# Performance work log

Hardware: AMD Instinct MI355X
Metric: run time of the kernel (lower is better)

Reference implementation:

```python
import jax, jax.numpy as jnp
import numpy as np

N_CELL, N_NET, N_GCELL = 50000, 10000, 20000
E = 100000
D = 32   # hidden_node = hidden_net = hidden_hanna = out_node = out_net
DP = 16  # hidden_pin = hidden_edge feats


def setup_inputs() -> dict:
    key = jax.random.key(0)
    ks = jax.random.split(key, 21)
    f = jax.random.normal
    ri = lambda k, n: jax.random.randint(k, (E,), 0, n, dtype=jnp.int32)
    return {
        'node_feat': f(ks[0], (N_CELL, D), jnp.float32),
        'net_feat': f(ks[1], (N_NET, D), jnp.float32),
        'pin_feat': f(ks[2], (E, DP), jnp.float32),
        'hanna_feat': f(ks[3], (N_GCELL, D), jnp.float32),
        'edge_feat': f(ks[4], (E, DP), jnp.float32),
        'pins_src': ri(ks[5], N_CELL), 'pins_dst': ri(ks[6], N_NET),
        'pinned_src': ri(ks[7], N_NET), 'pinned_dst': ri(ks[8], N_CELL),
        'connect_src': ri(ks[9], N_GCELL), 'connect_dst': ri(ks[10], N_GCELL),
        'pt_src': ri(ks[11], N_CELL), 'pt_dst': ri(ks[12], N_GCELL),
        'pf_src': ri(ks[13], N_GCELL), 'pf_dst': ri(ks[14], N_CELL),
        'W_net': f(ks[15], (D, D)) * 0.1, 'b_net': jnp.zeros((D,), jnp.float32),
        'W_topo': f(ks[16], (DP, D * D)) * 0.1, 'b_topo': jnp.zeros((D * D,), jnp.float32),
        'W_pins': f(ks[17], (D, D)) * 0.1, 'b_pins': jnp.zeros((D,), jnp.float32),
        'W_connect': f(ks[18], (D, D)) * 0.1, 'b_connect': jnp.zeros((D,), jnp.float32),
        'W_pt': f(ks[19], (D, D)) * 0.1, 'b_pt': jnp.zeros((D,), jnp.float32),
        'b_pinned': jnp.zeros((D,), jnp.float32), 'b_pf': jnp.zeros((D,), jnp.float32),
    }


def _deg(idx, n):
    # clamped degree, as DGL clamps to min 1
    return jnp.maximum(jax.ops.segment_sum(jnp.ones_like(idx, jnp.float32), idx, n), 1.0)


def graph_conv(h_src, W, b, src, dst, n_src, n_dst):
    # DGL GraphConv with norm='both': D_out^{-1/2} gather -> sum -> D_in^{-1/2}, then W, b
    feat = (h_src * _deg(src, n_src)[:, None] ** -0.5) @ W
    agg = jax.ops.segment_sum(feat[src], dst, n_dst)
    return agg * _deg(dst, n_dst)[:, None] ** -0.5 + b


def nn_conv(h_src, efeat, W_topo, b_topo, bias, src, dst, n_dst):
    # DGL NNConv (aggregator='mean'): per-edge weight from edge_func, mean over in-edges
    d_in = h_src.shape[1]
    w = (efeat @ W_topo + b_topo).reshape(-1, d_in, bias.shape[0])  # (E, d_in, d_out)
    m = jnp.einsum('ei,eio->eo', h_src[src], w)
    return jax.ops.segment_sum(m, dst, n_dst) / _deg(dst, n_dst)[:, None] + bias


def reference(node_feat, net_feat, pin_feat, hanna_feat, edge_feat,
              pins_src, pins_dst, pinned_src, pinned_dst, connect_src, connect_dst,
              pt_src, pt_dst, pf_src, pf_dst,
              W_net, b_net, W_topo, b_topo, W_pins, b_pins,
              W_connect, b_connect, W_pt, b_pt, b_pinned, b_pf):
    # 'pins': cell -> net (GraphConv)
    h_net = graph_conv(node_feat, W_pins, b_pins, pins_src, pins_dst, N_CELL, N_NET)
    # 'pinned': net -> cell (NNConv) + 'point-from': gcell -> cell (NNConv); agg='sum'
    h_cell = (nn_conv(net_feat, pin_feat, W_topo, b_topo, b_pinned, pinned_src, pinned_dst, N_CELL)
              + nn_conv(hanna_feat, edge_feat, W_topo, b_topo, b_pf, pf_src, pf_dst, N_CELL))
    # 'connect': gcell -> gcell + 'point-to': cell -> gcell (GraphConvs); agg='sum'
    h_gcell = (graph_conv(hanna_feat, W_connect, b_connect, connect_src, connect_dst, N_GCELL, N_GCELL)
               + graph_conv(node_feat, W_pt, b_pt, pt_src, pt_dst, N_CELL, N_GCELL))
    return (h_cell, h_net + net_feat @ W_net + b_net, h_gcell)
```

## Files before the change

kernel.cpp:

```cpp
#include <hip/hip_runtime.h>

typedef unsigned short u16;
typedef unsigned int u32;

#define NC 50000
#define NN 10000
#define NG 20000
#define NE 100000
#define NSCAN 150016
#define NBLK 74


__device__ __forceinline__ float bflo(u32 a) { return __uint_as_float(a << 16); }
__device__ __forceinline__ float bfhi(u32 a) { return __uint_as_float(a & 0xFFFF0000u); }
__device__ __forceinline__ u16 fbf(float f) {
  u32 u = __float_as_uint(f);
  return (u16)((u + 0x7FFFu + ((u >> 16) & 1u)) >> 16);
}

__device__ __forceinline__ float nn_msg(int e, int s, const float* __restrict__ ef,
                                        const u16* __restrict__ T,
                                        const float* __restrict__ C, int o) {
  const float4* efp = reinterpret_cast<const float4*>(ef + (size_t)e * 16);
  float4 ea = efp[0], eb = efp[1], ec = efp[2], ed = efp[3];
  const uint4* tp = reinterpret_cast<const uint4*>(T + (size_t)s * 512 + o * 16);
  uint4 ta = tp[0], tb = tp[1];
  float m = C[(size_t)s * 32 + o];
  m += ea.x * bflo(ta.x) + ea.y * bfhi(ta.x) + ea.z * bflo(ta.y) + ea.w * bfhi(ta.y);
  m += eb.x * bflo(ta.z) + eb.y * bfhi(ta.z) + eb.z * bflo(ta.w) + eb.w * bfhi(ta.w);
  m += ec.x * bflo(tb.x) + ec.y * bfhi(tb.x) + ec.z * bflo(tb.y) + ec.w * bfhi(tb.y);
  m += ed.x * bflo(tb.z) + ed.y * bfhi(tb.z) + ed.z * bflo(tb.w) + ed.w * bfhi(tb.w);
  return m;
}

__global__ __launch_bounds__(512) void k_front(
    const float* __restrict__ feat_net, const float* __restrict__ feat_han,
    const float* __restrict__ W_topo, const float* __restrict__ b_topo,
    u16* __restrict__ T_net, u16* __restrict__ T_han,
    float* __restrict__ C_net, float* __restrict__ C_han,
    const int* __restrict__ pins_src, const int* __restrict__ pins_dst,
    const int* __restrict__ pinned_dst, const int* __restrict__ pf_dst,
    const int* __restrict__ connect_src, const int* __restrict__ connect_dst,
    const int* __restrict__ pt_src, const int* __restrict__ pt_dst,
    int* __restrict__ hist, int* __restrict__ srccnt) {
  int b = blockIdx.x;
  if (b < 938) {
    bool han = b >= 313;
    const float* feat = han ? feat_han : feat_net;
    u16* T = han ? T_han : T_net;
    int n = han ? NG : NN;
    int blk = han ? b - 313 : b;
    int j = threadIdx.x;
    int p = j & 15, o = j >> 4;
    float w[32];
#pragma unroll
    for (int i = 0; i < 32; i++) w[i] = W_topo[p * 1024 + i * 32 + o];
    int s0 = blk * 32;
    int s1 = min(s0 + 32, n);
    int sn = s0;
    for (; sn + 1 < s1; sn += 2) {
      const float* h0 = feat + (size_t)sn * 32;
      const float* h1 = h0 + 32;
      float a0 = 0.f, a1 = 0.f;
#pragma unroll
      for (int i = 0; i < 32; i++) {
        a0 += h0[i] * w[i];
        a1 += h1[i] * w[i];
      }
      T[(size_t)sn * 512 + j] = fbf(a0);
      T[(size_t)(sn + 1) * 512 + j] = fbf(a1);
    }
    if (sn < s1) {
      const float* h0 = feat + (size_t)sn * 32;
      float a0 = 0.f;
#pragma unroll
      for (int i = 0; i < 32; i++) a0 += h0[i] * w[i];
      T[(size_t)sn * 512 + j] = fbf(a0);
    }
    return;
  }
  if (b < 2813) {
    int t = (b - 938) * 512 + threadIdx.x;
    int s2 = t >> 5, o = t & 31;
    bool han = s2 >= NN;
    const float* feat = han ? feat_han : feat_net;
    float* C = han ? C_han : C_net;
    int s = han ? s2 - NN : s2;
    float acc = 0.f;
#pragma unroll 8
    for (int i = 0; i < 32; i++)
      acc += feat[(size_t)s * 32 + i] * b_topo[i * 32 + o];
    C[(size_t)s * 32 + o] = acc;
    return;
  }
  int e = (b - 2813) * 512 + threadIdx.x;
  if (e >= NE) return;
  atomicAdd(&hist[pins_dst[e]], 1);
  atomicAdd(&hist[10000 + connect_dst[e]], 1);
  atomicAdd(&hist[30000 + pt_dst[e]], 1);
  atomicAdd(&hist[50000 + pinned_dst[e]], 1);
  atomicAdd(&hist[100000 + pf_dst[e]], 1);
  atomicAdd(&srccnt[pins_src[e]], 1);
  atomicAdd(&srccnt[50000 + connect_src[e]], 1);
  atomicAdd(&srccnt[70000 + pt_src[e]], 1);
}

__global__ __launch_bounds__(256) void k_scan1(
    const int* __restrict__ cnt, int* __restrict__ bsum) {
  __shared__ int sm[256];
  int b = blockIdx.x, tid = threadIdx.x;
  int base = b * 2048 + tid * 8;
  int tot = 0;
#pragma unroll
  for (int j = 0; j < 8; j++) {
    int i = base + j;
    tot += (i < NSCAN) ? cnt[i] : 0;
  }
  sm[tid] = tot;
  __syncthreads();
  for (int off = 128; off > 0; off >>= 1) {
    if (tid < off) sm[tid] += sm[tid + off];
    __syncthreads();
  }
  if (tid == 0) bsum[b] = sm[0];
}

__global__ __launch_bounds__(256) void k_scan3(
    const int* __restrict__ cnt, const int* __restrict__ bsum,
    int* __restrict__ bases) {
  __shared__ int sm[256];
  __shared__ int carry;
  int b = blockIdx.x, tid = threadIdx.x;
  if (tid == 0) {
    int run = 0;
    for (int i = 0; i < NBLK; i++) {
      if (i == b) break;
      run += bsum[i];
    }
    carry = run;
  }
  int base = b * 2048 + tid * 8;
  int v[8];
  int tot = 0;
#pragma unroll
  for (int j = 0; j < 8; j++) {
    int i = base + j;
    v[j] = (i < NSCAN) ? cnt[i] : 0;
    tot += v[j];
  }
  sm[tid] = tot;
  __syncthreads();
  for (int off = 1; off < 256; off <<= 1) {
    int add = (tid >= off) ? sm[tid - off] : 0;
    __syncthreads();
    sm[tid] += add;
    __syncthreads();
  }
  int excl = sm[tid] - tot + carry;
#pragma unroll
  for (int j = 0; j < 8; j++) {
    int i = base + j;
    if (i < NSCAN) bases[i] = excl;
    excl += v[j];
  }
}

__global__ __launch_bounds__(512) void k_fill(
    const int* __restrict__ pins_dst, const int* __restrict__ connect_dst,
    const int* __restrict__ pt_dst, const int* __restrict__ pinned_dst,
    const int* __restrict__ pf_dst,
    const int* __restrict__ bases, int* __restrict__ cursor,
    int* __restrict__ idx_all) {
  int t = blockIdx.x * 512 + threadIdx.x;
  if (t >= 5 * NE) return;
  int r = t / NE, e = t - r * NE;
  const int* dsts = r == 0 ? pins_dst : r == 1 ? connect_dst
                   : r == 2 ? pt_dst : r == 3 ? pinned_dst : pf_dst;
  int off = r == 0 ? 0 : r == 1 ? 10000 : r == 2 ? 30000 : r == 3 ? 50000 : 100000;
  int g = off + dsts[e];
  int pos = atomicAdd(&cursor[g], 1);
  idx_all[bases[g] + pos] = e;
}

__global__ __launch_bounds__(512) void k_gc_gather(
    const int* __restrict__ hist, const int* __restrict__ bases,
    const int* __restrict__ idx_all, const int* __restrict__ srccnt,
    const int* __restrict__ pins_src, const int* __restrict__ connect_src,
    const int* __restrict__ pt_src,
    const float* __restrict__ node_feat, const float* __restrict__ hanna_feat,
    float* __restrict__ S_net, float* __restrict__ S_conn, float* __restrict__ S_pt) {
  int t = blockIdx.x * 512 + threadIdx.x;
  int rr = t >> 5, o = t & 31;
  int rel = (rr >= 10000) + (rr >= 30000);
  const int* srcarr = rel == 0 ? pins_src : rel == 1 ? connect_src : pt_src;
  const float* feat = (rel == 1) ? hanna_feat : node_feat;
  const int* scnt = srccnt + (rel == 0 ? 0 : rel == 1 ? 50000 : 70000);
  float* S = rel == 0 ? S_net + (size_t)rr * 32
           : rel == 1 ? S_conn + (size_t)(rr - 10000) * 32
                      : S_pt + (size_t)(rr - 30000) * 32;
  int base = bases[rr], deg = hist[rr];
  float acc = 0.f;
  int k = 0;
  for (; k + 1 < deg; k += 2) {
    int ea = idx_all[base + k], eb = idx_all[base + k + 1];
    int sa = srcarr[ea], sb = srcarr[eb];
    float wa = rsqrtf(fmaxf((float)scnt[sa], 1.f));
    float wb = rsqrtf(fmaxf((float)scnt[sb], 1.f));
    acc += feat[(size_t)sa * 32 + o] * wa + feat[(size_t)sb * 32 + o] * wb;
  }
  if (k < deg) {
    int e = idx_all[base + k];
    int s = srcarr[e];
    acc += feat[(size_t)s * 32 + o] * rsqrtf(fmaxf((float)scnt[s], 1.f));
  }
  S[o] = acc;
}

__global__ __launch_bounds__(512) void k_tail(
    const int* __restrict__ hist, const int* __restrict__ bases,
    const int* __restrict__ idx_all,
    const int* __restrict__ pinned_src, const int* __restrict__ pf_src,
    const float* __restrict__ pin_feat, const float* __restrict__ edge_feat,
    const u16* __restrict__ T_net, const u16* __restrict__ T_han,
    const float* __restrict__ C_net, const float* __restrict__ C_han,
    const float* __restrict__ b_pinned, const float* __restrict__ b_pf,
    const float* __restrict__ S_net, const float* __restrict__ net_feat,
    const float* __restrict__ W_pins, const float* __restrict__ b_pins,
    const float* __restrict__ W_net, const float* __restrict__ b_net,
    const float* __restrict__ S_conn, const float* __restrict__ S_pt,
    const float* __restrict__ W_connect, const float* __restrict__ b_connect,
    const float* __restrict__ W_pt, const float* __restrict__ b_pt,
    float* __restrict__ out) {
  __shared__ float Wa[1024], Wb[1024];
  int b = blockIdx.x;
  if (b < 3125) {
    int t = b * 512 + threadIdx.x;
    int d = t >> 5, o = t & 31;
    float a0 = 0.f, a1 = 0.f;
    {
      int g = 50000 + d;
      int base = bases[g], deg = hist[g];
      int k = 0;
      for (; k + 1 < deg; k += 2) {
        int ea = idx_all[base + k], eb = idx_all[base + k + 1];
        int sa = pinned_src[ea], sb = pinned_src[eb];
        a0 += nn_msg(ea, sa, pin_feat, T_net, C_net, o) +
              nn_msg(eb, sb, pin_feat, T_net, C_net, o);
      }
      if (k < deg) {
        int e = idx_all[base + k];
        a0 += nn_msg(e, pinned_src[e], pin_feat, T_net, C_net, o);
      }
      a0 /= fmaxf((float)deg, 1.f);
    }
    {
      int g = 100000 + d;
      int base = bases[g], deg = hist[g];
      int k = 0;
      for (; k + 1 < deg; k += 2) {
        int ea = idx_all[base + k], eb = idx_all[base + k + 1];
        int sa = pf_src[ea], sb = pf_src[eb];
        a1 += nn_msg(ea, sa, edge_feat, T_han, C_han, o) +
              nn_msg(eb, sb, edge_feat, T_han, C_han, o);
      }
      if (k < deg) {
        int e = idx_all[base + k];
        a1 += nn_msg(e, pf_src[e], edge_feat, T_han, C_han, o);
      }
      a1 /= fmaxf((float)deg, 1.f);
    }
    out[(size_t)d * 32 + o] = a0 + a1 + b_pinned[o] + b_pf[o];
    return;
  }
  if (b < 3750) {
    for (int k = threadIdx.x; k < 1024; k += 512) {
      Wa[k] = W_pins[k];
      Wb[k] = W_net[k];
    }
    __syncthreads();
    int t = (b - 3125) * 512 + threadIdx.x;
    int r = t >> 5, o = t & 31;
    float a1 = 0.f, a2 = 0.f;
#pragma unroll 8
    for (int i = 0; i < 32; i++) {
      a1 += S_net[(size_t)r * 32 + i] * Wa[i * 32 + o];
      a2 += net_feat[(size_t)r * 32 + i] * Wb[i * 32 + o];
    }
    out[1600000 + t] = a1 * rsqrtf(fmaxf((float)hist[r], 1.f)) + b_pins[o] +
                       a2 + b_net[o];
    return;
  }
  for (int k = threadIdx.x; k < 1024; k += 512) {
    Wa[k] = W_connect[k];
    Wb[k] = W_pt[k];
  }
  __syncthreads();
  int t = (b - 3750) * 512 + threadIdx.x;
  int r = t >> 5, o = t & 31;
  float a1 = 0.f, a2 = 0.f;
#pragma unroll 8
  for (int i = 0; i < 32; i++) {
    a1 += S_conn[(size_t)r * 32 + i] * Wa[i * 32 + o];
    a2 += S_pt[(size_t)r * 32 + i] * Wb[i * 32 + o];
  }
  out[1920000 + t] = a1 * rsqrtf(fmaxf((float)hist[10000 + r], 1.f)) + b_connect[o] +
                     a2 * rsqrtf(fmaxf((float)hist[30000 + r], 1.f)) + b_pt[o];
}

extern "C" void kernel_launch(void* const* d_in, const int* in_sizes, int n_in,
                              void* d_out, int out_size, void* d_ws, size_t ws_size,
                              hipStream_t stream) {
  const float* node_feat  = (const float*)d_in[0];
  const float* net_feat   = (const float*)d_in[1];
  const float* pin_feat   = (const float*)d_in[2];
  const float* hanna_feat = (const float*)d_in[3];
  const float* edge_feat  = (const float*)d_in[4];
  const int* pins_src    = (const int*)d_in[5];
  const int* pins_dst    = (const int*)d_in[6];
  const int* pinned_src  = (const int*)d_in[7];
  const int* pinned_dst  = (const int*)d_in[8];
  const int* connect_src = (const int*)d_in[9];
  const int* connect_dst = (const int*)d_in[10];
  const int* pt_src      = (const int*)d_in[11];
  const int* pt_dst      = (const int*)d_in[12];
  const int* pf_src      = (const int*)d_in[13];
  const int* pf_dst      = (const int*)d_in[14];
  const float* W_net     = (const float*)d_in[15];
  const float* b_net     = (const float*)d_in[16];
  const float* W_topo    = (const float*)d_in[17];
  const float* b_topo    = (const float*)d_in[18];
  const float* W_pins    = (const float*)d_in[19];
  const float* b_pins    = (const float*)d_in[20];
  const float* W_connect = (const float*)d_in[21];
  const float* b_connect = (const float*)d_in[22];
  const float* W_pt      = (const float*)d_in[23];
  const float* b_pt      = (const float*)d_in[24];
  const float* b_pinned  = (const float*)d_in[25];
  const float* b_pf      = (const float*)d_in[26];
  float* out = (float*)d_out;

  int* wi = (int*)d_ws;
  int* hist    = wi + 0;
  int* cursor  = wi + 150016;
  int* srccnt  = wi + 300032;
  int* bases   = wi + 420032;
  int* bsum    = wi + 570064;
  int* idx_all = wi + 570192;
  float* wf = (float*)d_ws;
  float* S_net  = wf + 1070192;
  float* S_conn = wf + 1390192;
  float* S_pt   = wf + 2030192;
  float* C_net  = wf + 2670192;
  float* C_han  = wf + 2990192;
  u16* T_net = (u16*)((char*)d_ws + 14520832);
  u16* T_han = (u16*)((char*)d_ws + 14520832 + 10240000);

  hipMemsetAsync(d_ws, 0, 420032 * sizeof(int), stream);

  k_front<<<3009, 512, 0, stream>>>(
      net_feat, hanna_feat, W_topo, b_topo, T_net, T_han, C_net, C_han,
      pins_src, pins_dst, pinned_dst, pf_dst, connect_src, connect_dst,
      pt_src, pt_dst, hist, srccnt);

  k_scan1<<<NBLK, 256, 0, stream>>>(hist, bsum);
  k_scan3<<<NBLK, 256, 0, stream>>>(hist, bsum, bases);

  k_fill<<<(5 * NE + 511) / 512, 512, 0, stream>>>(
      pins_dst, connect_dst, pt_dst, pinned_dst, pf_dst, bases, cursor, idx_all);

  k_gc_gather<<<3125, 512, 0, stream>>>(
      hist, bases, idx_all, srccnt, pins_src, connect_src, pt_src,
      node_feat, hanna_feat, S_net, S_conn, S_pt);

  k_tail<<<5000, 512, 0, stream>>>(
      hist, bases, idx_all, pinned_src, pf_src, pin_feat, edge_feat,
      T_net, T_han, C_net, C_han, b_pinned, b_pf,
      S_net, net_feat, W_pins, b_pins, W_net, b_net,
      S_conn, S_pt, W_connect, b_connect, W_pt, b_pt, out);
}
```

Before: 303.9 us.

## Store source ids and norm weights in CSR; tile topo transform through shared memory

The fill kernel now writes CSR entries as int2 pairs, with the source index and a precomputed rsqrt degree weight for GraphConv relations, and edge id plus source for NNConv relations. This removes the dependent idx→src→srccnt gather chains in the gather and tail kernels. The topo-transform front blocks stage 64 feature rows in shared memory, compute two outputs per thread and write packed bf16 pairs, which cuts the block count. In exchange the CSR doubles in size, the fill kernel does more work, and the workspace layout is shifted.

```diff
diff --git a/kernel.cpp b/kernel.cpp
--- a/kernel.cpp
+++ b/kernel.cpp
@@ -44,43 +44,55 @@
     const int* __restrict__ pt_src, const int* __restrict__ pt_dst,
     int* __restrict__ hist, int* __restrict__ srccnt) {
   int b = blockIdx.x;
-  if (b < 938) {
-    bool han = b >= 313;
-    const float* feat = han ? feat_han : feat_net;
-    u16* T = han ? T_han : T_net;
-    int n = han ? NG : NN;
-    int blk = han ? b - 313 : b;
-    int j = threadIdx.x;
-    int p = j & 15, o = j >> 4;
-    float w[32];
-#pragma unroll
-    for (int i = 0; i < 32; i++) w[i] = W_topo[p * 1024 + i * 32 + o];
-    int s0 = blk * 32;
-    int s1 = min(s0 + 32, n);
-    int sn = s0;
-    for (; sn + 1 < s1; sn += 2) {
-      const float* h0 = feat + (size_t)sn * 32;
-      const float* h1 = h0 + 32;
+  int tid = threadIdx.x;
+  if (b < 469) {
+    __shared__ float hs[64][32];
+    int nd0 = b * 64;
+    {
+      int idx = tid * 4;
+      int nl = idx >> 5, i = idx & 31;
+      int ng = nd0 + nl;
+      int ngc = min(ng, 29999);
+      const float* rp = (ngc < NN) ? feat_net + (size_t)ngc * 32
+                                   : feat_han + (size_t)(ngc - NN) * 32;
+      *reinterpret_cast<float4*>(&hs[nl][i]) =
+          *reinterpret_cast<const float4*>(rp + i);
+    }
+    int jj = tid & 255;
+    int j0 = jj * 2, j1 = j0 + 1;
+    int p0 = j0 & 15, o0 = j0 >> 4;
+    int p1 = j1 & 15, o1 = j1 >> 4;
+    float w0[32], w1[32];
+#pragma unroll
+    for (int i = 0; i < 32; i++) {
+      w0[i] = W_topo[p0 * 1024 + i * 32 + o0];
+      w1[i] = W_topo[p1 * 1024 + i * 32 + o1];
+    }
+    __syncthreads();
+    int g = tid >> 8;
+#pragma unroll 4
+    for (int n = 0; n < 32; n++) {
+      int nl = g * 32 + n;
       float a0 = 0.f, a1 = 0.f;
 #pragma unroll
       for (int i = 0; i < 32; i++) {
-        a0 += h0[i] * w[i];
-        a1 += h1[i] * w[i];
-      }
-      T[(size_t)sn * 512 + j] = fbf(a0);
-      T[(size_t)(sn + 1) * 512 + j] = fbf(a1);
-    }
-    if (sn < s1) {
-      const float* h0 = feat + (size_t)sn * 32;
-      float a0 = 0.f;
-#pragma unroll
-      for (int i = 0; i < 32; i++) a0 += h0[i] * w[i];
-      T[(size_t)sn * 512 + j] = fbf(a0);
+        float h = hs[nl][i];
+        a0 += h * w0[i];
+        a1 += h * w1[i];
+      }
+      int s = nd0 + nl;
+      if (s < 30000) {
+        u32 pk = (u32)fbf(a0) | ((u32)fbf(a1) << 16);
+        u32* dst = (s < NN)
+            ? reinterpret_cast<u32*>(T_net + (size_t)s * 512 + j0)
+            : reinterpret_cast<u32*>(T_han + (size_t)(s - NN) * 512 + j0);
+        *dst = pk;
+      }
     }
     return;
   }
-  if (b < 2813) {
-    int t = (b - 938) * 512 + threadIdx.x;
+  if (b < 2344) {
+    int t = (b - 469) * 512 + tid;
     int s2 = t >> 5, o = t & 31;
     bool han = s2 >= NN;
     const float* feat = han ? feat_han : feat_net;
@@ -93,7 +105,7 @@
     C[(size_t)s * 32 + o] = acc;
     return;
   }
-  int e = (b - 2813) * 512 + threadIdx.x;
+  int e = (b - 2344) * 512 + tid;
   if (e >= NE) return;
   atomicAdd(&hist[pins_dst[e]], 1);
   atomicAdd(&hist[10000 + connect_dst[e]], 1);
@@ -133,10 +145,7 @@
   int b = blockIdx.x, tid = threadIdx.x;
   if (tid == 0) {
     int run = 0;
-    for (int i = 0; i < NBLK; i++) {
-      if (i == b) break;
-      run += bsum[i];
-    }
+    for (int i = 0; i < b; i++) run += bsum[i];
     carry = run;
   }
   int base = b * 2048 + tid * 8;
@@ -166,35 +175,45 @@
 }
 
 __global__ __launch_bounds__(512) void k_fill(
-    const int* __restrict__ pins_dst, const int* __restrict__ connect_dst,
-    const int* __restrict__ pt_dst, const int* __restrict__ pinned_dst,
-    const int* __restrict__ pf_dst,
+    const int* __restrict__ pins_src, const int* __restrict__ pins_dst,
+    const int* __restrict__ connect_src, const int* __restrict__ connect_dst,
+    const int* __restrict__ pt_src, const int* __restrict__ pt_dst,
+    const int* __restrict__ pinned_src, const int* __restrict__ pinned_dst,
+    const int* __restrict__ pf_src, const int* __restrict__ pf_dst,
+    const int* __restrict__ srccnt,
     const int* __restrict__ bases, int* __restrict__ cursor,
-    int* __restrict__ idx_all) {
+    int2* __restrict__ csr_gc, int2* __restrict__ csr_nn) {
   int t = blockIdx.x * 512 + threadIdx.x;
   if (t >= 5 * NE) return;
-  int r = t / NE, e = t - r * NE;
+  int r = (t >= NE) + (t >= 2 * NE) + (t >= 3 * NE) + (t >= 4 * NE);
+  int e = t - r * NE;
+  const int* srcs = r == 0 ? pins_src : r == 1 ? connect_src
+                   : r == 2 ? pt_src : r == 3 ? pinned_src : pf_src;
   const int* dsts = r == 0 ? pins_dst : r == 1 ? connect_dst
                    : r == 2 ? pt_dst : r == 3 ? pinned_dst : pf_dst;
   int off = r == 0 ? 0 : r == 1 ? 10000 : r == 2 ? 30000 : r == 3 ? 50000 : 100000;
+  int s = srcs[e];
   int g = off + dsts[e];
   int pos = atomicAdd(&cursor[g], 1);
-  idx_all[bases[g] + pos] = e;
+  int cpos = bases[g] + pos;
+  if (r < 3) {
+    int soff = r == 0 ? 0 : r == 1 ? 50000 : 70000;
+    float w = rsqrtf(fmaxf((float)srccnt[soff + s], 1.f));
+    csr_gc[cpos] = make_int2(s, __float_as_int(w));
+  } else {
+    csr_nn[cpos - 300000] = make_int2(e, s);
+  }
 }
 
 __global__ __launch_bounds__(512) void k_gc_gather(
     const int* __restrict__ hist, const int* __restrict__ bases,
-    const int* __restrict__ idx_all, const int* __restrict__ srccnt,
-    const int* __restrict__ pins_src, const int* __restrict__ connect_src,
-    const int* __restrict__ pt_src,
+    const int2* __restrict__ csr_gc,
     const float* __restrict__ node_feat, const float* __restrict__ hanna_feat,
     float* __restrict__ S_net, float* __restrict__ S_conn, float* __restrict__ S_pt) {
   int t = blockIdx.x * 512 + threadIdx.x;
   int rr = t >> 5, o = t & 31;
   int rel = (rr >= 10000) + (rr >= 30000);
-  const int* srcarr = rel == 0 ? pins_src : rel == 1 ? connect_src : pt_src;
   const float* feat = (rel == 1) ? hanna_feat : node_feat;
-  const int* scnt = srccnt + (rel == 0 ? 0 : rel == 1 ? 50000 : 70000);
   float* S = rel == 0 ? S_net + (size_t)rr * 32
            : rel == 1 ? S_conn + (size_t)(rr - 10000) * 32
                       : S_pt + (size_t)(rr - 30000) * 32;
@@ -202,24 +221,20 @@
   float acc = 0.f;
   int k = 0;
   for (; k + 1 < deg; k += 2) {
-    int ea = idx_all[base + k], eb = idx_all[base + k + 1];
-    int sa = srcarr[ea], sb = srcarr[eb];
-    float wa = rsqrtf(fmaxf((float)scnt[sa], 1.f));
-    float wb = rsqrtf(fmaxf((float)scnt[sb], 1.f));
-    acc += feat[(size_t)sa * 32 + o] * wa + feat[(size_t)sb * 32 + o] * wb;
+    int2 pa = csr_gc[base + k], pb = csr_gc[base + k + 1];
+    acc += feat[(size_t)pa.x * 32 + o] * __int_as_float(pa.y) +
+           feat[(size_t)pb.x * 32 + o] * __int_as_float(pb.y);
   }
   if (k < deg) {
-    int e = idx_all[base + k];
-    int s = srcarr[e];
-    acc += feat[(size_t)s * 32 + o] * rsqrtf(fmaxf((float)scnt[s], 1.f));
+    int2 pa = csr_gc[base + k];
+    acc += feat[(size_t)pa.x * 32 + o] * __int_as_float(pa.y);
   }
   S[o] = acc;
 }
 
 __global__ __launch_bounds__(512) void k_tail(
     const int* __restrict__ hist, const int* __restrict__ bases,
-    const int* __restrict__ idx_all,
-    const int* __restrict__ pinned_src, const int* __restrict__ pf_src,
+    const int2* __restrict__ csr_nn,
     const float* __restrict__ pin_feat, const float* __restrict__ edge_feat,
     const u16* __restrict__ T_net, const u16* __restrict__ T_han,
     const float* __restrict__ C_net, const float* __restrict__ C_han,
@@ -239,33 +254,31 @@
     float a0 = 0.f, a1 = 0.f;
     {
       int g = 50000 + d;
-      int base = bases[g], deg = hist[g];
+      int base = bases[g] - 300000, deg = hist[g];
       int k = 0;
       for (; k + 1 < deg; k += 2) {
-        int ea = idx_all[base + k], eb = idx_all[base + k + 1];
-        int sa = pinned_src[ea], sb = pinned_src[eb];
-        a0 += nn_msg(ea, sa, pin_feat, T_net, C_net, o) +
-              nn_msg(eb, sb, pin_feat, T_net, C_net, o);
+        int2 ea = csr_nn[base + k], eb = csr_nn[base + k + 1];
+        a0 += nn_msg(ea.x, ea.y, pin_feat, T_net, C_net, o) +
+              nn_msg(eb.x, eb.y, pin_feat, T_net, C_net, o);
       }
       if (k < deg) {
-        int e = idx_all[base + k];
-        a0 += nn_msg(e, pinned_src[e], pin_feat, T_net, C_net, o);
+        int2 ea = csr_nn[base + k];
+        a0 += nn_msg(ea.x, ea.y, pin_feat, T_net, C_net, o);
       }
       a0 /= fmaxf((float)deg, 1.f);
     }
     {
       int g = 100000 + d;
-      int base = bases[g], deg = hist[g];
+      int base = bases[g] - 300000, deg = hist[g];
       int k = 0;
       for (; k + 1 < deg; k += 2) {
-        int ea = idx_all[base + k], eb = idx_all[base + k + 1];
-        int sa = pf_src[ea], sb = pf_src[eb];
-        a1 += nn_msg(ea, sa, edge_feat, T_han, C_han, o) +
-              nn_msg(eb, sb, edge_feat, T_han, C_han, o);
+        int2 ea = csr_nn[base + k], eb = csr_nn[base + k + 1];
+        a1 += nn_msg(ea.x, ea.y, edge_feat, T_han, C_han, o) +
+              nn_msg(eb.x, eb.y, edge_feat, T_han, C_han, o);
       }
       if (k < deg) {
-        int e = idx_all[base + k];
-        a1 += nn_msg(e, pf_src[e], edge_feat, T_han, C_han, o);
+        int2 ea = csr_nn[base + k];
+        a1 += nn_msg(ea.x, ea.y, edge_feat, T_han, C_han, o);
       }
       a1 /= fmaxf((float)deg, 1.f);
     }
@@ -345,19 +358,20 @@
   int* srccnt  = wi + 300032;
   int* bases   = wi + 420032;
   int* bsum    = wi + 570064;
-  int* idx_all = wi + 570192;
+  int2* csr_gc = (int2*)(wi + 570192);
+  int2* csr_nn = (int2*)(wi + 1170192);
   float* wf = (float*)d_ws;
-  float* S_net  = wf + 1070192;
-  float* S_conn = wf + 1390192;
-  float* S_pt   = wf + 2030192;
-  float* C_net  = wf + 2670192;
-  float* C_han  = wf + 2990192;
-  u16* T_net = (u16*)((char*)d_ws + 14520832);
-  u16* T_han = (u16*)((char*)d_ws + 14520832 + 10240000);
+  float* S_net  = wf + 1570192;
+  float* S_conn = wf + 1890192;
+  float* S_pt   = wf + 2530192;
+  float* C_net  = wf + 3170192;
+  float* C_han  = wf + 3490192;
+  u16* T_net = (u16*)((char*)d_ws + 16520832);
+  u16* T_han = (u16*)((char*)d_ws + 16520832 + 10240000);
 
   hipMemsetAsync(d_ws, 0, 420032 * sizeof(int), stream);
 
-  k_front<<<3009, 512, 0, stream>>>(
+  k_front<<<2540, 512, 0, stream>>>(
       net_feat, hanna_feat, W_topo, b_topo, T_net, T_han, C_net, C_han,
       pins_src, pins_dst, pinned_dst, pf_dst, connect_src, connect_dst,
       pt_src, pt_dst, hist, srccnt);
@@ -366,14 +380,15 @@
   k_scan3<<<NBLK, 256, 0, stream>>>(hist, bsum, bases);
 
   k_fill<<<(5 * NE + 511) / 512, 512, 0, stream>>>(
-      pins_dst, connect_dst, pt_dst, pinned_dst, pf_dst, bases, cursor, idx_all);
+      pins_src, pins_dst, connect_src, connect_dst, pt_src, pt_dst,
+      pinned_src, pinned_dst, pf_src, pf_dst, srccnt, bases, cursor,
+      csr_gc, csr_nn);
 
   k_gc_gather<<<3125, 512, 0, stream>>>(
-      hist, bases, idx_all, srccnt, pins_src, connect_src, pt_src,
-      node_feat, hanna_feat, S_net, S_conn, S_pt);
+      hist, bases, csr_gc, node_feat, hanna_feat, S_net, S_conn, S_pt);
 
   k_tail<<<5000, 512, 0, stream>>>(
-      hist, bases, idx_all, pinned_src, pf_src, pin_feat, edge_feat,
+      hist, bases, csr_nn, pin_feat, edge_feat,
       T_net, T_han, C_net, C_han, b_pinned, b_pf,
       S_net, net_feat, W_pins, b_pins, W_net, b_net,
       S_conn, S_pt, W_connect, b_connect, W_pt, b_pt, out);
```

After: 283.6 us. 1.07x faster.
